# Optimization experiments

Measured on AMD Instinct MI355X. Metric: run time of the kernel, lower is better.

The kernel has to match this reference:

```python
import jax, jax.numpy as jnp
import numpy as np

D_STATE = 16
D_CONV = 4
DT_RANK = 16  # ceil(d_model/16) = ceil(256/16)
N_LAYERS = 2
EPS = 1e-5


def _layernorm(x, g, b):
    m = jnp.mean(x, -1, keepdims=True)
    v = jnp.var(x, -1, keepdims=True)
    return (x - m) * jax.lax.rsqrt(v + EPS) * g + b


def _causal_conv(x, w, b):
    # x [B,L,D], depthwise causal conv, w [D,K], b [D]
    K = w.shape[1]
    L = x.shape[1]
    xp = jnp.pad(x, ((0, 0), (K - 1, 0), (0, 0)))
    y = sum(xp[:, k:k + L, :] * w[:, k] for k in range(K))
    return y + b


def _selective_scan(u, dt, A, Bm, Cm, D_skip):
    # u, dt [B,L,d]; A [d,n]; Bm, Cm [B,L,n]; D_skip [d]
    def step(h, inp):
        dt_t, B_t, C_t, u_t = inp  # [B,d],[B,n],[B,n],[B,d]
        dA = jnp.exp(dt_t[:, :, None] * A)                      # [B,d,n]
        h = dA * h + dt_t[:, :, None] * B_t[:, None, :] * u_t[:, :, None]
        y = jnp.einsum('bdn,bn->bd', h, C_t)
        return h, y

    Bsz, L, d = u.shape
    h0 = jnp.zeros((Bsz, d, A.shape[1]), u.dtype)
    xs = (dt.transpose(1, 0, 2), Bm.transpose(1, 0, 2),
          Cm.transpose(1, 0, 2), u.transpose(1, 0, 2))
    _, ys = jax.lax.scan(step, h0, xs)                          # [L,B,d]
    return ys.transpose(1, 0, 2) + u * D_skip


def _mamba_block(x, Wip, cw, cb, Wxp, Wdt, bdt, Alog, Dp, Wout):
    xz = x @ Wip                                                # [B,L,2*d_inner]
    d_inner = Wip.shape[1] // 2
    xc, z = xz[..., :d_inner], xz[..., d_inner:]
    xc = jax.nn.silu(_causal_conv(xc, cw, cb))
    xdbl = xc @ Wxp                                             # [B,L,dt_rank+2n]
    dt = jax.nn.softplus(xdbl[..., :DT_RANK] @ Wdt + bdt)
    Bm = xdbl[..., DT_RANK:DT_RANK + D_STATE]
    Cm = xdbl[..., DT_RANK + D_STATE:]
    A = -jnp.exp(Alog)
    y = _selective_scan(xc, dt, A, Bm, Cm, Dp)
    y = y * jax.nn.silu(z)
    return y @ Wout


def reference(z_t, W_in, b_in, ln_g, ln_b, W_inproj, conv_w, conv_b, W_xproj,
              W_dt, b_dt, A_log, D_skip, W_out, W_outp, b_outp, lno_g, lno_b):
    x = z_t @ W_in + b_in                                       # [B,L,d_model]
    for i in range(N_LAYERS):
        res = x
        xn = _layernorm(x, ln_g[i], ln_b[i])
        x = res + _mamba_block(xn, W_inproj[i], conv_w[i], conv_b[i],
                               W_xproj[i], W_dt[i], b_dt[i], A_log[i],
                               D_skip[i], W_out[i])  # dropout is identity in eval
    u = x @ W_outp + b_outp
    return _layernorm(u, lno_g, lno_b)


def setup_inputs() -> dict:
    key = jax.random.key(0)
    B, L = 16, 2048
    d_input, d_model, d_output, d_inner = 1088, 256, 64, 512
    n = N_LAYERS
    ks = jax.random.split(key, 10)

    def rn(k, shape, fan):
        return jax.random.normal(k, shape, jnp.float32) / np.float32(np.sqrt(fan))

    A_init = jnp.log(jnp.arange(1, D_STATE + 1, dtype=jnp.float32))
    return {
        'z_t': jax.random.normal(ks[0], (B, L, d_input), jnp.float32),
        'W_in': rn(ks[1], (d_input, d_model), d_input),
        'b_in': jnp.zeros((d_model,), jnp.float32),
        'ln_g': jnp.ones((n, d_model), jnp.float32),
        'ln_b': jnp.zeros((n, d_model), jnp.float32),
        'W_inproj': rn(ks[2], (n, d_model, 2 * d_inner), d_model),
        'conv_w': rn(ks[3], (n, d_inner, D_CONV), D_CONV),
        'conv_b': jnp.zeros((n, d_inner), jnp.float32),
        'W_xproj': rn(ks[4], (n, d_inner, DT_RANK + 2 * D_STATE), d_inner),
        'W_dt': rn(ks[5], (n, DT_RANK, d_inner), DT_RANK),
        'b_dt': jnp.full((n, d_inner), -4.6, jnp.float32),  # softplus ~ 0.01
        'A_log': jnp.broadcast_to(A_init, (n, d_inner, D_STATE)) + 0.0,
        'D_skip': jnp.ones((n, d_inner), jnp.float32),
        'W_out': rn(ks[6], (n, d_inner, d_model), d_inner),
        'W_outp': rn(ks[7], (d_model, d_output), d_model),
        'b_outp': jnp.zeros((d_output,), jnp.float32),
        'lno_g': jnp.ones((d_output,), jnp.float32),
        'lno_b': jnp.zeros((d_output,), jnp.float32),
    }
```

## Files before the change

kernel.cpp:

```cpp
#include <hip/hip_runtime.h>
#include <hip/hip_bf16.h>
#include <math.h>
#include <stdint.h>

#define L_SEQ 2048
#define BATCH 16
#define NROWS (BATCH * L_SEQ)
#define DMODEL 256
#define DINNER 512
#define C_CH 32
#define T_CH 64
#define LOG2E 1.4426950408889634f

typedef __attribute__((ext_vector_type(8))) __bf16 bf16x8;
typedef __attribute__((ext_vector_type(4))) float f32x4;
typedef __attribute__((ext_vector_type(8))) unsigned short u16x8;
typedef __attribute__((address_space(1))) const uint32_t gu32;
typedef __attribute__((address_space(3))) uint32_t lu32;

#if __has_builtin(__builtin_amdgcn_exp2f)
#define EXP2F __builtin_amdgcn_exp2f
#else
#define EXP2F exp2f
#endif

__device__ __forceinline__ float sigmoidf_(float x) { return 1.f / (1.f + __expf(-x)); }

__device__ __forceinline__ unsigned short f2bf(float f) {
    union { float f; uint32_t u; } v; v.f = f;
    uint32_t r = v.u + 0x7FFF + ((v.u >> 16) & 1);
    return (unsigned short)(r >> 16);
}
__device__ __forceinline__ float bf2f(unsigned short h) {
    union { uint32_t u; float f; } v; v.u = ((uint32_t)h) << 16;
    return v.f;
}

__device__ __forceinline__ void gld16(const void* g, void* l) {
    __builtin_amdgcn_global_load_lds((gu32*)g, (lu32*)l, 16, 0, 0);
}

template <int N> __device__ __forceinline__ void waitv() {
    if constexpr (N == 0)       asm volatile("s_waitcnt vmcnt(0)" ::: "memory");
    else if constexpr (N == 3)  asm volatile("s_waitcnt vmcnt(3)" ::: "memory");
    else if constexpr (N == 4)  asm volatile("s_waitcnt vmcnt(4)" ::: "memory");
    else if constexpr (N == 6)  asm volatile("s_waitcnt vmcnt(6)" ::: "memory");
    else if constexpr (N == 8)  asm volatile("s_waitcnt vmcnt(8)" ::: "memory");
    else if constexpr (N == 16) asm volatile("s_waitcnt vmcnt(16)" ::: "memory");
}

__global__ __launch_bounds__(256) void wtrans(const float* __restrict__ W,
                                              unsigned short* __restrict__ Wt, int K, int N) {
    int idx = blockIdx.x * 256 + threadIdx.x;
    if (idx < K * N) {
        int n = idx / K, k = idx % K;
        Wt[idx] = f2bf(W[(size_t)k * N + n]);
    }
}
__global__ __launch_bounds__(256) void wtrans_pad(const float* __restrict__ W,
                                                  unsigned short* __restrict__ Wt,
                                                  int K, int Nreal, int Npad) {
    int idx = blockIdx.x * 256 + threadIdx.x;
    if (idx < Npad * K) {
        int n = idx / K, k = idx % K;
        Wt[idx] = (n < Nreal) ? f2bf(W[(size_t)k * Nreal + n]) : (unsigned short)0;
    }
}

template <int TM, int TN, int BK, bool A_F32, bool HAS_BIAS, bool HAS_RES, bool OUT_BF16>
__global__ __launch_bounds__(256) void gemm_bf16(
    const void* __restrict__ Aptr, const unsigned short* __restrict__ Bt,
    const float* __restrict__ bias, const float* __restrict__ res,
    void* __restrict__ Cout, int M, int N, int K, int Nout)
{
    constexpr int MR = TM / 32;
    constexpr int NR = TN / 32;
    constexpr int EWA = A_F32 ? 4 : 2;
    constexpr int RBA = BK * EWA;
    constexpr int RBB = BK * 2;
    constexpr int ABYTES = TM * RBA;
    constexpr int BBYTES = TN * RBB;
    constexpr int OPSA = ABYTES / 4096;
    constexpr int OPSB = BBYTES / 4096;
    constexpr int VOPS = OPSA + OPSB;
    constexpr bool SWZA = (RBA >= 128);
    constexpr bool SWZB = (RBB >= 128);
    constexpr int KK = BK / 32;
    __shared__ __align__(16) char Alds[2][ABYTES];
    __shared__ __align__(16) char Blds[2][BBYTES];
    const int tid = threadIdx.x;
    const int w = tid >> 6, lane = tid & 63;

    const int nwg = gridDim.x;
    const int q = nwg >> 3;
    const int wg = (blockIdx.x & 7) * q + (blockIdx.x >> 3);
    const int nx = N / TN;
    const int bm = (wg / nx) * TM, bn = (wg % nx) * TN;

    const int wr = (w >> 1) * (TM / 2), wc = (w & 1) * (TN / 2);
    const int fr = lane & 15, fq = lane >> 4;
    const size_t KbB = (size_t)K * 2;
    const size_t KbA = (size_t)K * EWA;

    const char* Ab = (const char*)Aptr;
    const char* Bb = (const char*)Bt;
    const int lds0 = w * 1024;

    f32x4 acc[MR][NR];
#pragma unroll
    for (int m = 0; m < MR; m++)
#pragma unroll
        for (int n = 0; n < NR; n++) acc[m][n] = (f32x4){0.f, 0.f, 0.f, 0.f};

    auto stageA = [&](int buf, int k0) {
        char* lA = Alds[buf];
#pragma unroll
        for (int i = 0; i < OPSA; i++) {
            const int o = i * 4096 + tid * 16;
            const int row = o / RBA;
            int col = o % RBA;
            if constexpr (SWZA) col ^= (row & 7) << 4;
            gld16(Ab + (size_t)(bm + row) * KbA + (size_t)k0 * EWA + col,
                  lA + i * 4096 + lds0);
        }
    };
    auto stageB = [&](int buf, int k0) {
        char* lB = Blds[buf];
#pragma unroll
        for (int i = 0; i < OPSB; i++) {
            const int o = i * 4096 + tid * 16;
            const int row = o / RBB;
            int col = o % RBB;
            if constexpr (SWZB) col ^= (row & 7) << 4;
            gld16(Bb + (size_t)(bn + row) * KbB + (size_t)k0 * 2 + col,
                  lB + i * 4096 + lds0);
        }
    };
    auto compute = [&](int buf) {
        const char* lA = Alds[buf];
        const char* lB = Blds[buf];
#pragma unroll
        for (int kk = 0; kk < KK; kk++) {
            bf16x8 af[MR], bg[NR];
#pragma unroll
            for (int m = 0; m < MR; m++) {
                const int row = wr + m * 16 + fr;
                const int sw = SWZA ? ((row & 7) << 4) : 0;
                if constexpr (A_F32) {
                    const int b0 = row * RBA + kk * 128 + fq * 32;
                    float4 x0 = *(const float4*)(lA + (b0 ^ sw));
                    float4 x1 = *(const float4*)(lA + ((b0 + 16) ^ sw));
                    bf16x8 a;
                    a[0]=(__bf16)x0.x; a[1]=(__bf16)x0.y; a[2]=(__bf16)x0.z; a[3]=(__bf16)x0.w;
                    a[4]=(__bf16)x1.x; a[5]=(__bf16)x1.y; a[6]=(__bf16)x1.z; a[7]=(__bf16)x1.w;
                    af[m] = a;
                } else {
                    const int c = kk * 64 + fq * 16;
                    af[m] = *(const bf16x8*)(lA + row * RBA + (c ^ sw));
                }
            }
#pragma unroll
            for (int n = 0; n < NR; n++) {
                const int row = wc + n * 16 + fr;
                const int sw = SWZB ? ((row & 7) << 4) : 0;
                const int c = kk * 64 + fq * 16;
                bg[n] = *(const bf16x8*)(lB + row * RBB + (c ^ sw));
            }
#pragma unroll
            for (int m = 0; m < MR; m++)
#pragma unroll
                for (int n = 0; n < NR; n++)
                    acc[m][n] = __builtin_amdgcn_mfma_f32_16x16x32_bf16(af[m], bg[n], acc[m][n], 0, 0, 0);
        }
    };

    const int NT = K / BK;

    stageA(0, 0); stageB(0, 0);
    asm volatile("s_waitcnt vmcnt(0) lgkmcnt(0)" ::: "memory");
    __builtin_amdgcn_s_barrier();
    __builtin_amdgcn_sched_barrier(0);

    for (int kt = 0; kt < NT; ++kt) {
        const int cur = kt & 1;
        const bool has_next = (kt + 1 < NT);
        if (has_next) {
            const int k0 = (kt + 1) * BK;
            stageA(cur ^ 1, k0); stageB(cur ^ 1, k0);
            waitv<VOPS>();
        } else {
            waitv<0>();
        }
        __builtin_amdgcn_s_barrier();
        __builtin_amdgcn_sched_barrier(0);

        compute(cur);

        asm volatile("s_waitcnt lgkmcnt(0)" ::: "memory");
        __builtin_amdgcn_s_barrier();
        __builtin_amdgcn_sched_barrier(0);
    }

#pragma unroll
    for (int m = 0; m < MR; m++) {
#pragma unroll
        for (int n = 0; n < NR; n++) {
            int col = bn + wc + n * 16 + fr;
            if (col < Nout) {
#pragma unroll
                for (int r = 0; r < 4; r++) {
                    int row = bm + wr + m * 16 + fq * 4 + r;
                    float v = acc[m][n][r];
                    if (HAS_BIAS) v += bias[col];
                    if (HAS_RES)  v += res[(size_t)row * Nout + col];
                    if (OUT_BF16) ((unsigned short*)Cout)[(size_t)row * Nout + col] = f2bf(v);
                    else          ((float*)Cout)[(size_t)row * Nout + col] = v;
                }
            }
        }
    }
}

__global__ __launch_bounds__(256) void ln256(
    const float* __restrict__ x, const float* __restrict__ g,
    const float* __restrict__ b, unsigned short* __restrict__ out)
{
    int lane = threadIdx.x & 63, wid = threadIdx.x >> 6;
    size_t r = (size_t)blockIdx.x * 4 + wid;
    const float4 v = *(const float4*)&x[r * 256 + lane * 4];
    float s = v.x + v.y + v.z + v.w;
    float sq = v.x * v.x + v.y * v.y + v.z * v.z + v.w * v.w;
#pragma unroll
    for (int off = 32; off; off >>= 1) { s += __shfl_xor(s, off); sq += __shfl_xor(sq, off); }
    float mean = s * (1.f / 256.f);
    float var = sq * (1.f / 256.f) - mean * mean;
    float rs = rsqrtf(var + 1e-5f);
    float4 gv = *(const float4*)&g[lane * 4];
    float4 bv = *(const float4*)&b[lane * 4];
    ushort4 o;
    o.x = f2bf((v.x - mean) * rs * gv.x + bv.x);
    o.y = f2bf((v.y - mean) * rs * gv.y + bv.y);
    o.z = f2bf((v.z - mean) * rs * gv.z + bv.z);
    o.w = f2bf((v.w - mean) * rs * gv.w + bv.w);
    *(ushort4*)&out[r * 256 + lane * 4] = o;
}

__global__ __launch_bounds__(256) void ln64(
    const float* __restrict__ t, const float* __restrict__ g,
    const float* __restrict__ b, float* __restrict__ out)
{
    int lane = threadIdx.x & 63, wid = threadIdx.x >> 6;
    size_t r = (size_t)blockIdx.x * 4 + wid;
    float v = t[r * 64 + lane];
    float s = v, sq = v * v;
#pragma unroll
    for (int off = 32; off; off >>= 1) { s += __shfl_xor(s, off); sq += __shfl_xor(sq, off); }
    float mean = s * (1.f / 64.f);
    float var = sq * (1.f / 64.f) - mean * mean;
    out[r * 64 + lane] = (v - mean) * rsqrtf(var + 1e-5f) * g[lane] + b[lane];
}

__global__ __launch_bounds__(256) void conv_silu8(
    const unsigned short* __restrict__ xz, const float* __restrict__ w,
    const float* __restrict__ cb, unsigned short* __restrict__ xc)
{
    int idx = blockIdx.x * 256 + threadIdx.x;
    int d8 = (idx & 63) << 3;
    int l  = (idx >> 6) & 2047;
    int b  = idx >> 17;
    const unsigned short* base = xz + ((size_t)b * L_SEQ + l) * 1024 + d8;
    u16x8 t0 = {0,0,0,0,0,0,0,0}, t1 = t0, t2 = t0;
    u16x8 t3 = *(const u16x8*)base;
    if (l >= 1) t2 = *(const u16x8*)(base - 1024);
    if (l >= 2) t1 = *(const u16x8*)(base - 2048);
    if (l >= 3) t0 = *(const u16x8*)(base - 3072);
    u16x8 o;
#pragma unroll
    for (int j = 0; j < 8; j++) {
        float4 wv = *(const float4*)&w[(d8 + j) * 4];
        float acc = cb[d8 + j];
        acc = fmaf(bf2f(t0[j]), wv.x, acc);
        acc = fmaf(bf2f(t1[j]), wv.y, acc);
        acc = fmaf(bf2f(t2[j]), wv.z, acc);
        acc = fmaf(bf2f(t3[j]), wv.w, acc);
        o[j] = f2bf(acc * sigmoidf_(acc));
    }
    *(u16x8*)&xc[((size_t)b * L_SEQ + l) * 512 + d8] = o;
}

__global__ __launch_bounds__(256) void scan_pass1(
    const unsigned short* __restrict__ xc, const float* __restrict__ xdbl,
    const float* __restrict__ Wdt, const float* __restrict__ bdt,
    const float* __restrict__ Alog,
    float* __restrict__ Tbuf, float* __restrict__ Sbuf)
{
    __shared__ float xs[T_CH][32];
    int idx = blockIdx.x * 256 + threadIdx.x;
    int d = idx & 511;
    int c = (idx >> 9) & (C_CH - 1);
    int b = idx >> 14;
    size_t r0 = (size_t)b * L_SEQ + (size_t)c * T_CH;
#pragma unroll
    for (int ii = 0; ii < 2; ii++) {
        int i = threadIdx.x + ii * 256, row = i >> 3, qq = i & 7;
        *(float4*)&xs[row][qq * 4] = *(const float4*)&xdbl[(r0 + row) * 48 + qq * 4];
    }
    __syncthreads();

    float wdt[16];
#pragma unroll
    for (int j = 0; j < 16; j++) wdt[j] = Wdt[j * 512 + d];
    const float bd = bdt[d];

    float a[16], a2[16], S[16];
#pragma unroll
    for (int n = 0; n < 16; n++) a[n] = -__expf(Alog[d * 16 + n]);
#pragma unroll
    for (int n = 0; n < 16; n++) a2[n] = a[n] * LOG2E;
#pragma unroll
    for (int n = 0; n < 16; n++) S[n] = 0.f;
    bool pow_ok = true;
#pragma unroll
    for (int n = 1; n < 16; n++)
        pow_ok = pow_ok && (fabsf(a[n] - (n + 1) * a[0]) <= 1e-3f * (n + 1) * fabsf(a[0]));
    const float a0l2 = a[0] * LOG2E;
    float Tsum = 0.f;

    if (pow_ok) {
        for (int t = 0; t < T_CH; t++) {
            float dtr = bd;
#pragma unroll
            for (int j = 0; j < 16; j++) dtr = fmaf(xs[t][j], wdt[j], dtr);
            float dtv = (dtr > 20.f) ? dtr : __logf(1.f + __expf(dtr));
            float u = bf2f(xc[(r0 + t) * 512 + d]);
            float dtu = dtv * u;
            Tsum += dtv;
            float e1 = EXP2F(dtv * a0l2), e2 = e1 * e1;
            S[0] = fmaf(e1, S[0], dtu * xs[t][16]);
            S[1] = fmaf(e2, S[1], dtu * xs[t][17]);
            float pm2 = e1, pm1 = e2;
#pragma unroll
            for (int n = 2; n < 16; n++) {
                float cur = pm2 * e2;
                S[n] = fmaf(cur, S[n], dtu * xs[t][16 + n]);
                pm2 = pm1; pm1 = cur;
            }
        }
    } else {
        for (int t = 0; t < T_CH; t++) {
            float dtr = bd;
#pragma unroll
            for (int j = 0; j < 16; j++) dtr = fmaf(xs[t][j], wdt[j], dtr);
            float dtv = (dtr > 20.f) ? dtr : __logf(1.f + __expf(dtr));
            float u = bf2f(xc[(r0 + t) * 512 + d]);
            float dtu = dtv * u;
            Tsum += dtv;
#pragma unroll
            for (int n = 0; n < 16; n++) {
                float dA = EXP2F(dtv * a2[n]);
                S[n] = fmaf(dA, S[n], dtu * xs[t][16 + n]);
            }
        }
    }
    Tbuf[idx] = Tsum;
    size_t o = (size_t)idx * 16;
#pragma unroll
    for (int qq = 0; qq < 4; qq++)
        *(float4*)&Sbuf[o + qq * 4] = make_float4(S[qq*4], S[qq*4+1], S[qq*4+2], S[qq*4+3]);
}

__global__ __launch_bounds__(256) void scan_pass2(
    const float* __restrict__ Tbuf, const float* __restrict__ Alog,
    float* __restrict__ Sbuf)
{
    int g = blockIdx.x * 256 + threadIdx.x;
    int nd = g & 8191;
    int b = g >> 13;
    int d = nd >> 4, n = nd & 15;
    const float a2 = -__expf(Alog[d * 16 + n]) * LOG2E;
    float H = 0.f;
    for (int c = 0; c < C_CH; c++) {
        size_t base = (size_t)(b * C_CH + c);
        float T = Tbuf[base * 512 + d];
        float P = EXP2F(T * a2);
        size_t idx = base * 8192 + nd;
        float S = Sbuf[idx];
        float Hn = fmaf(P, H, S);
        Sbuf[idx] = H;
        H = Hn;
    }
}

__global__ __launch_bounds__(256) void scan_pass3(
    const unsigned short* __restrict__ xcin, const unsigned short* __restrict__ xz,
    const float* __restrict__ xdbl, const float* __restrict__ Wdt,
    const float* __restrict__ bdt, const float* __restrict__ Alog,
    const float* __restrict__ Dsk, const float* __restrict__ Sbuf,
    unsigned short* __restrict__ y)
{
    __shared__ float xs[T_CH][48];
    int idx = blockIdx.x * 256 + threadIdx.x;
    int d = idx & 511;
    int c = (idx >> 9) & (C_CH - 1);
    int b = idx >> 14;
    size_t r0 = (size_t)b * L_SEQ + (size_t)c * T_CH;
#pragma unroll
    for (int ii = 0; ii < 3; ii++) {
        int i = threadIdx.x + ii * 256, row = i / 12, qq = i % 12;
        *(float4*)&xs[row][qq * 4] = *(const float4*)&xdbl[(r0 + row) * 48 + qq * 4];
    }
    __syncthreads();

    float wdt[16];
#pragma unroll
    for (int j = 0; j < 16; j++) wdt[j] = Wdt[j * 512 + d];
    const float bd = bdt[d];

    float a[16], a2[16], h[16];
#pragma unroll
    for (int n = 0; n < 16; n++) a[n] = -__expf(Alog[d * 16 + n]);
#pragma unroll
    for (int n = 0; n < 16; n++) a2[n] = a[n] * LOG2E;
    {
        size_t o = (size_t)idx * 16;
#pragma unroll
        for (int qq = 0; qq < 4; qq++) {
            float4 v = *(const float4*)&Sbuf[o + qq * 4];
            h[qq*4] = v.x; h[qq*4+1] = v.y; h[qq*4+2] = v.z; h[qq*4+3] = v.w;
        }
    }
    bool pow_ok = true;
#pragma unroll
    for (int n = 1; n < 16; n++)
        pow_ok = pow_ok && (fabsf(a[n] - (n + 1) * a[0]) <= 1e-3f * (n + 1) * fabsf(a[0]));
    const float a0l2 = a[0] * LOG2E;
    const float Dv = Dsk[d];

    if (pow_ok) {
        for (int t = 0; t < T_CH; t++) {
            size_t ridx = (r0 + t) * 512 + d;
            float dtr = bd;
#pragma unroll
            for (int j = 0; j < 16; j++) dtr = fmaf(xs[t][j], wdt[j], dtr);
            float dtv = (dtr > 20.f) ? dtr : __logf(1.f + __expf(dtr));
            float u = bf2f(xcin[ridx]);
            float dtu = dtv * u;
            float e1 = EXP2F(dtv * a0l2), e2 = e1 * e1;
            float yv = 0.f;
            h[0] = fmaf(e1, h[0], dtu * xs[t][16]);  yv = fmaf(h[0], xs[t][32], yv);
            h[1] = fmaf(e2, h[1], dtu * xs[t][17]);  yv = fmaf(h[1], xs[t][33], yv);
            float pm2 = e1, pm1 = e2;
#pragma unroll
            for (int n = 2; n < 16; n++) {
                float cur = pm2 * e2;
                h[n] = fmaf(cur, h[n], dtu * xs[t][16 + n]);
                yv = fmaf(h[n], xs[t][32 + n], yv);
                pm2 = pm1; pm1 = cur;
            }
            yv = fmaf(u, Dv, yv);
            float z = bf2f(xz[(r0 + t) * 1024 + 512 + d]);
            y[ridx] = f2bf(yv * z * sigmoidf_(z));
        }
    } else {
        for (int t = 0; t < T_CH; t++) {
            size_t ridx = (r0 + t) * 512 + d;
            float dtr = bd;
#pragma unroll
            for (int j = 0; j < 16; j++) dtr = fmaf(xs[t][j], wdt[j], dtr);
            float dtv = (dtr > 20.f) ? dtr : __logf(1.f + __expf(dtr));
            float u = bf2f(xcin[ridx]);
            float dtu = dtv * u;
            float yv = 0.f;
#pragma unroll
            for (int n = 0; n < 16; n++) {
                float dA = EXP2F(dtv * a2[n]);
                h[n] = fmaf(dA, h[n], dtu * xs[t][16 + n]);
                yv = fmaf(h[n], xs[t][32 + n], yv);
            }
            yv = fmaf(u, Dv, yv);
            float z = bf2f(xz[(r0 + t) * 1024 + 512 + d]);
            y[ridx] = f2bf(yv * z * sigmoidf_(z));
        }
    }
}

extern "C" void kernel_launch(void* const* d_in, const int* in_sizes, int n_in,
                              void* d_out, int out_size, void* d_ws, size_t ws_size,
                              hipStream_t stream)
{
    const float* z_t     = (const float*)d_in[0];
    const float* W_in    = (const float*)d_in[1];
    const float* b_in    = (const float*)d_in[2];
    const float* ln_g    = (const float*)d_in[3];
    const float* ln_b    = (const float*)d_in[4];
    const float* W_inpr  = (const float*)d_in[5];
    const float* conv_w  = (const float*)d_in[6];
    const float* conv_b  = (const float*)d_in[7];
    const float* W_xproj = (const float*)d_in[8];
    const float* W_dt    = (const float*)d_in[9];
    const float* b_dt    = (const float*)d_in[10];
    const float* A_log   = (const float*)d_in[11];
    const float* D_skip  = (const float*)d_in[12];
    const float* W_out   = (const float*)d_in[13];
    const float* W_outp  = (const float*)d_in[14];
    const float* b_outp  = (const float*)d_in[15];
    const float* lno_g   = (const float*)d_in[16];
    const float* lno_b   = (const float*)d_in[17];
    float* out           = (float*)d_out;

    char* p = (char*)d_ws;
    float*          x    = (float*)p;          p += (size_t)NROWS * DMODEL * 4;
    unsigned short* xn   = (unsigned short*)p; p += (size_t)NROWS * DMODEL * 2;
    unsigned short* xc   = (unsigned short*)p; p += (size_t)NROWS * DINNER * 2;
    unsigned short* xz   = (unsigned short*)p; p += (size_t)NROWS * 1024 * 2;
    float*          xdbl = (float*)p;          p += (size_t)NROWS * 48 * 4;
    float*          Pregion = (float*)p;       p += (size_t)BATCH * C_CH * DINNER * 16 * 4;
    float*          Sbuf = (float*)p;          p += (size_t)BATCH * C_CH * DINNER * 16 * 4;
    unsigned short* WinT  = (unsigned short*)p; p += (size_t)256 * 1088 * 2;
    unsigned short* WipT  = (unsigned short*)p; p += (size_t)2 * 1024 * 256 * 2;
    unsigned short* WoutT = (unsigned short*)p; p += (size_t)2 * 256 * 512 * 2;
    unsigned short* WxpT  = (unsigned short*)p; p += (size_t)2 * 128 * 512 * 2;
    unsigned short* WopT  = (unsigned short*)p; p += (size_t)128 * 256 * 2;
    float* Tbuf = Pregion;
    float* otmp = Pregion;

    wtrans<<<(256 * 1088 + 255) / 256, 256, 0, stream>>>(W_in, WinT, 1088, 256);
    for (int l = 0; l < 2; l++) {
        wtrans<<<(1024 * 256 + 255) / 256, 256, 0, stream>>>(
            W_inpr + (size_t)l * 256 * 1024, WipT + (size_t)l * 1024 * 256, 256, 1024);
        wtrans<<<(256 * 512 + 255) / 256, 256, 0, stream>>>(
            W_out + (size_t)l * 512 * 256, WoutT + (size_t)l * 256 * 512, 512, 256);
        wtrans_pad<<<(128 * 512 + 255) / 256, 256, 0, stream>>>(
            W_xproj + (size_t)l * 512 * 48, WxpT + (size_t)l * 128 * 512, 512, 48, 128);
    }
    wtrans_pad<<<(128 * 256 + 255) / 256, 256, 0, stream>>>(W_outp, WopT, 256, 64, 128);

    gemm_bf16<64, 128, 64, true, true, false, false><<<(NROWS / 64) * (256 / 128), 256, 0, stream>>>(
        z_t, WinT, b_in, nullptr, x, NROWS, 256, 1088, 256);

    for (int layer = 0; layer < 2; ++layer) {
        ln256<<<NROWS / 4, 256, 0, stream>>>(x, ln_g + layer * 256, ln_b + layer * 256, xn);
        gemm_bf16<128, 256, 32, false, false, false, true><<<(NROWS / 128) * (1024 / 256), 256, 0, stream>>>(
            xn, WipT + (size_t)layer * 1024 * 256, nullptr, nullptr, xz, NROWS, 1024, 256, 1024);
        conv_silu8<<<NROWS * 64 / 256, 256, 0, stream>>>(
            xz, conv_w + layer * 512 * 4, conv_b + layer * 512, xc);
        gemm_bf16<64, 128, 64, false, false, false, false><<<(NROWS / 64) * (128 / 128), 256, 0, stream>>>(
            xc, WxpT + (size_t)layer * 128 * 512, nullptr, nullptr, xdbl, NROWS, 128, 512, 48);

        const float* Al_l  = A_log + layer * 512 * 16;
        const float* Wdt_l = W_dt + layer * 16 * 512;
        const float* bdt_l = b_dt + layer * 512;
        scan_pass1<<<BATCH * C_CH * DINNER / 256, 256, 0, stream>>>(
            xc, xdbl, Wdt_l, bdt_l, Al_l, Tbuf, Sbuf);
        scan_pass2<<<BATCH * DINNER * 16 / 256, 256, 0, stream>>>(Tbuf, Al_l, Sbuf);
        scan_pass3<<<BATCH * C_CH * DINNER / 256, 256, 0, stream>>>(
            xc, xz, xdbl, Wdt_l, bdt_l, Al_l, D_skip + layer * 512, Sbuf, xc);

        if (layer == 0) {
            gemm_bf16<64, 128, 64, false, false, true, false><<<(NROWS / 64) * (256 / 128), 256, 0, stream>>>(
                xc, WoutT, nullptr, x, x, NROWS, 256, 512, 256);
        } else {
            gemm_bf16<64, 128, 64, false, false, true, true><<<(NROWS / 64) * (256 / 128), 256, 0, stream>>>(
                xc, WoutT + (size_t)256 * 512, nullptr, x, xn, NROWS, 256, 512, 256);
        }
    }

    gemm_bf16<64, 128, 32, false, true, false, false><<<(NROWS / 64) * (128 / 128), 256, 0, stream>>>(
        xn, WopT, b_outp, nullptr, otmp, NROWS, 128, 256, 64);
    ln64<<<NROWS / 4, 256, 0, stream>>>(otmp, lno_g, lno_b, out);
}
```

Baseline: 577.7 us.

## Fuse weight transposes, fold output LayerNorm into final GEMM, retile in-proj

Combines the eight weight transpose/convert launches into one kernel that dispatches on block index. Fuses the final LayerNorm over 64 channels into the epilogue of the output projection GEMM, reducing across lanes with shuffles, so the intermediate tensor is no longer written and re-read. Changes the in-projection GEMM tile from 128x256 to 128x128, which doubles the number of blocks. This saves launches and memory traffic, but the fused epilogue leaves half the waves idle during the LN step (only wc==0 waves work).

```diff
diff --git a/kernel.cpp b/kernel.cpp
--- a/kernel.cpp
+++ b/kernel.cpp
@@ -49,29 +49,48 @@
     else if constexpr (N == 16) asm volatile("s_waitcnt vmcnt(16)" ::: "memory");
 }
 
-__global__ __launch_bounds__(256) void wtrans(const float* __restrict__ W,
-                                              unsigned short* __restrict__ Wt, int K, int N) {
-    int idx = blockIdx.x * 256 + threadIdx.x;
-    if (idx < K * N) {
-        int n = idx / K, k = idx % K;
-        Wt[idx] = f2bf(W[(size_t)k * N + n]);
-    }
-}
-__global__ __launch_bounds__(256) void wtrans_pad(const float* __restrict__ W,
-                                                  unsigned short* __restrict__ Wt,
-                                                  int K, int Nreal, int Npad) {
-    int idx = blockIdx.x * 256 + threadIdx.x;
-    if (idx < Npad * K) {
-        int n = idx / K, k = idx % K;
-        Wt[idx] = (n < Nreal) ? f2bf(W[(size_t)k * Nreal + n]) : (unsigned short)0;
-    }
-}
-
-template <int TM, int TN, int BK, bool A_F32, bool HAS_BIAS, bool HAS_RES, bool OUT_BF16>
+__global__ __launch_bounds__(256) void wtrans_all(
+    const float* __restrict__ W_in, const float* __restrict__ W_inpr,
+    const float* __restrict__ W_out, const float* __restrict__ W_xproj,
+    const float* __restrict__ W_outp,
+    unsigned short* __restrict__ WinT, unsigned short* __restrict__ WipT,
+    unsigned short* __restrict__ WoutT, unsigned short* __restrict__ WxpT,
+    unsigned short* __restrict__ WopT)
+{
+    const int bid = blockIdx.x, tid = threadIdx.x;
+    if (bid < 1088) {
+        int idx = bid * 256 + tid;
+        int n = idx / 1088, k = idx % 1088;
+        WinT[idx] = f2bf(W_in[(size_t)k * 256 + n]);
+    } else if (bid < 3136) {
+        int l = (bid - 1088) >> 10;
+        int idx = ((bid - 1088) & 1023) * 256 + tid;
+        int n = idx >> 8, k = idx & 255;
+        WipT[(size_t)l * 262144 + idx] = f2bf(W_inpr[(size_t)l * 262144 + (size_t)k * 1024 + n]);
+    } else if (bid < 4160) {
+        int l = (bid - 3136) >> 9;
+        int idx = ((bid - 3136) & 511) * 256 + tid;
+        int n = idx >> 9, k = idx & 511;
+        WoutT[(size_t)l * 131072 + idx] = f2bf(W_out[(size_t)l * 131072 + (size_t)k * 256 + n]);
+    } else if (bid < 4672) {
+        int l = (bid - 4160) >> 8;
+        int idx = ((bid - 4160) & 255) * 256 + tid;
+        int n = idx >> 9, k = idx & 511;
+        WxpT[(size_t)l * 65536 + idx] =
+            (n < 48) ? f2bf(W_xproj[(size_t)l * (512 * 48) + (size_t)k * 48 + n]) : (unsigned short)0;
+    } else {
+        int idx = (bid - 4672) * 256 + tid;
+        int n = idx >> 8, k = idx & 255;
+        WopT[idx] = (n < 64) ? f2bf(W_outp[(size_t)k * 64 + n]) : (unsigned short)0;
+    }
+}
+
+template <int TM, int TN, int BK, bool A_F32, bool HAS_BIAS, bool HAS_RES, bool OUT_BF16, bool LN64OUT>
 __global__ __launch_bounds__(256) void gemm_bf16(
     const void* __restrict__ Aptr, const unsigned short* __restrict__ Bt,
     const float* __restrict__ bias, const float* __restrict__ res,
-    void* __restrict__ Cout, int M, int N, int K, int Nout)
+    void* __restrict__ Cout, int M, int N, int K, int Nout,
+    const float* __restrict__ lng, const float* __restrict__ lnb)
 {
     constexpr int MR = TM / 32;
     constexpr int NR = TN / 32;
@@ -201,20 +220,48 @@
         __builtin_amdgcn_sched_barrier(0);
     }
 
-#pragma unroll
-    for (int m = 0; m < MR; m++) {
-#pragma unroll
-        for (int n = 0; n < NR; n++) {
-            int col = bn + wc + n * 16 + fr;
-            if (col < Nout) {
+    if constexpr (LN64OUT) {
+        if (wc == 0) {
+#pragma unroll
+            for (int m = 0; m < MR; m++) {
 #pragma unroll
                 for (int r = 0; r < 4; r++) {
+                    float v[NR]; float s = 0.f, sq = 0.f;
+#pragma unroll
+                    for (int n = 0; n < NR; n++) {
+                        v[n] = acc[m][n][r] + bias[n * 16 + fr];
+                        s += v[n]; sq += v[n] * v[n];
+                    }
+#pragma unroll
+                    for (int off = 8; off; off >>= 1) { s += __shfl_xor(s, off); sq += __shfl_xor(sq, off); }
+                    float mean = s * (1.f / 64.f);
+                    float var = sq * (1.f / 64.f) - mean * mean;
+                    float rs = rsqrtf(var + 1e-5f);
                     int row = bm + wr + m * 16 + fq * 4 + r;
-                    float v = acc[m][n][r];
-                    if (HAS_BIAS) v += bias[col];
-                    if (HAS_RES)  v += res[(size_t)row * Nout + col];
-                    if (OUT_BF16) ((unsigned short*)Cout)[(size_t)row * Nout + col] = f2bf(v);
-                    else          ((float*)Cout)[(size_t)row * Nout + col] = v;
+#pragma unroll
+                    for (int n = 0; n < NR; n++) {
+                        int col = n * 16 + fr;
+                        ((float*)Cout)[(size_t)row * 64 + col] = (v[n] - mean) * rs * lng[col] + lnb[col];
+                    }
+                }
+            }
+        }
+    } else {
+#pragma unroll
+        for (int m = 0; m < MR; m++) {
+#pragma unroll
+            for (int n = 0; n < NR; n++) {
+                int col = bn + wc + n * 16 + fr;
+                if (col < Nout) {
+#pragma unroll
+                    for (int r = 0; r < 4; r++) {
+                        int row = bm + wr + m * 16 + fq * 4 + r;
+                        float v = acc[m][n][r];
+                        if (HAS_BIAS) v += bias[col];
+                        if (HAS_RES)  v += res[(size_t)row * Nout + col];
+                        if (OUT_BF16) ((unsigned short*)Cout)[(size_t)row * Nout + col] = f2bf(v);
+                        else          ((float*)Cout)[(size_t)row * Nout + col] = v;
+                    }
                 }
             }
         }
@@ -243,21 +290,6 @@
     o.z = f2bf((v.z - mean) * rs * gv.z + bv.z);
     o.w = f2bf((v.w - mean) * rs * gv.w + bv.w);
     *(ushort4*)&out[r * 256 + lane * 4] = o;
-}
-
-__global__ __launch_bounds__(256) void ln64(
-    const float* __restrict__ t, const float* __restrict__ g,
-    const float* __restrict__ b, float* __restrict__ out)
-{
-    int lane = threadIdx.x & 63, wid = threadIdx.x >> 6;
-    size_t r = (size_t)blockIdx.x * 4 + wid;
-    float v = t[r * 64 + lane];
-    float s = v, sq = v * v;
-#pragma unroll
-    for (int off = 32; off; off >>= 1) { s += __shfl_xor(s, off); sq += __shfl_xor(sq, off); }
-    float mean = s * (1.f / 64.f);
-    float var = sq * (1.f / 64.f) - mean * mean;
-    out[r * 64 + lane] = (v - mean) * rsqrtf(var + 1e-5f) * g[lane] + b[lane];
 }
 
 __global__ __launch_bounds__(256) void conv_silu8(
@@ -522,30 +554,21 @@
     unsigned short* WxpT  = (unsigned short*)p; p += (size_t)2 * 128 * 512 * 2;
     unsigned short* WopT  = (unsigned short*)p; p += (size_t)128 * 256 * 2;
     float* Tbuf = Pregion;
-    float* otmp = Pregion;
-
-    wtrans<<<(256 * 1088 + 255) / 256, 256, 0, stream>>>(W_in, WinT, 1088, 256);
-    for (int l = 0; l < 2; l++) {
-        wtrans<<<(1024 * 256 + 255) / 256, 256, 0, stream>>>(
-            W_inpr + (size_t)l * 256 * 1024, WipT + (size_t)l * 1024 * 256, 256, 1024);
-        wtrans<<<(256 * 512 + 255) / 256, 256, 0, stream>>>(
-            W_out + (size_t)l * 512 * 256, WoutT + (size_t)l * 256 * 512, 512, 256);
-        wtrans_pad<<<(128 * 512 + 255) / 256, 256, 0, stream>>>(
-            W_xproj + (size_t)l * 512 * 48, WxpT + (size_t)l * 128 * 512, 512, 48, 128);
-    }
-    wtrans_pad<<<(128 * 256 + 255) / 256, 256, 0, stream>>>(W_outp, WopT, 256, 64, 128);
-
-    gemm_bf16<64, 128, 64, true, true, false, false><<<(NROWS / 64) * (256 / 128), 256, 0, stream>>>(
-        z_t, WinT, b_in, nullptr, x, NROWS, 256, 1088, 256);
+
+    wtrans_all<<<4800, 256, 0, stream>>>(W_in, W_inpr, W_out, W_xproj, W_outp,
+                                         WinT, WipT, WoutT, WxpT, WopT);
+
+    gemm_bf16<64, 128, 64, true, true, false, false, false><<<(NROWS / 64) * (256 / 128), 256, 0, stream>>>(
+        z_t, WinT, b_in, nullptr, x, NROWS, 256, 1088, 256, nullptr, nullptr);
 
     for (int layer = 0; layer < 2; ++layer) {
         ln256<<<NROWS / 4, 256, 0, stream>>>(x, ln_g + layer * 256, ln_b + layer * 256, xn);
-        gemm_bf16<128, 256, 32, false, false, false, true><<<(NROWS / 128) * (1024 / 256), 256, 0, stream>>>(
-            xn, WipT + (size_t)layer * 1024 * 256, nullptr, nullptr, xz, NROWS, 1024, 256, 1024);
+        gemm_bf16<128, 128, 32, false, false, false, true, false><<<(NROWS / 128) * (1024 / 128), 256, 0, stream>>>(
+            xn, WipT + (size_t)layer * 1024 * 256, nullptr, nullptr, xz, NROWS, 1024, 256, 1024, nullptr, nullptr);
         conv_silu8<<<NROWS * 64 / 256, 256, 0, stream>>>(
             xz, conv_w + layer * 512 * 4, conv_b + layer * 512, xc);
-        gemm_bf16<64, 128, 64, false, false, false, false><<<(NROWS / 64) * (128 / 128), 256, 0, stream>>>(
-            xc, WxpT + (size_t)layer * 128 * 512, nullptr, nullptr, xdbl, NROWS, 128, 512, 48);
+        gemm_bf16<64, 128, 64, false, false, false, false, false><<<(NROWS / 64) * (128 / 128), 256, 0, stream>>>(
+            xc, WxpT + (size_t)layer * 128 * 512, nullptr, nullptr, xdbl, NROWS, 128, 512, 48, nullptr, nullptr);
 
         const float* Al_l  = A_log + layer * 512 * 16;
         const float* Wdt_l = W_dt + layer * 16 * 512;
@@ -557,15 +580,14 @@
             xc, xz, xdbl, Wdt_l, bdt_l, Al_l, D_skip + layer * 512, Sbuf, xc);
 
         if (layer == 0) {
-            gemm_bf16<64, 128, 64, false, false, true, false><<<(NROWS / 64) * (256 / 128), 256, 0, stream>>>(
-                xc, WoutT, nullptr, x, x, NROWS, 256, 512, 256);
+            gemm_bf16<64, 128, 64, false, false, true, false, false><<<(NROWS / 64) * (256 / 128), 256, 0, stream>>>(
+                xc, WoutT, nullptr, x, x, NROWS, 256, 512, 256, nullptr, nullptr);
         } else {
-            gemm_bf16<64, 128, 64, false, false, true, true><<<(NROWS / 64) * (256 / 128), 256, 0, stream>>>(
-                xc, WoutT + (size_t)256 * 512, nullptr, x, xn, NROWS, 256, 512, 256);
-        }
-    }
-
-    gemm_bf16<64, 128, 32, false, true, false, false><<<(NROWS / 64) * (128 / 128), 256, 0, stream>>>(
-        xn, WopT, b_outp, nullptr, otmp, NROWS, 128, 256, 64);
-    ln64<<<NROWS / 4, 256, 0, stream>>>(otmp, lno_g, lno_b, out);
-}
+            gemm_bf16<64, 128, 64, false, false, true, true, false><<<(NROWS / 64) * (256 / 128), 256, 0, stream>>>(
+                xc, WoutT + (size_t)256 * 512, nullptr, x, xn, NROWS, 256, 512, 256, nullptr, nullptr);
+        }
+    }
+
+    gemm_bf16<64, 128, 32, false, true, false, false, true><<<(NROWS / 64) * (128 / 128), 256, 0, stream>>>(
+        xn, WopT, b_outp, nullptr, out, NROWS, 128, 256, 64, lno_g, lno_b);
+}
```

Measured after the change: 530.6 us. -8.2%, faster.
